# Optimization experiments

Measured on AMD Instinct MI355X. Metric: run time of the kernel, lower is better.

The kernel has to match this reference:

```python
import jax, jax.numpy as jnp
import numpy as np

N, E, D = 100000, 400000, 128
LN_EPS = 1e-5
BN_EPS = 1e-5


def layer_norm(v, g, b):
    mu = jnp.mean(v, axis=-1, keepdims=True)
    var = jnp.var(v, axis=-1, keepdims=True)
    return (v - mu) * jax.lax.rsqrt(var + LN_EPS) * g + b


def setup_inputs() -> dict:
    key = jax.random.key(0)
    ks = jax.random.split(key, 12)
    s1 = 1.0 / np.sqrt(2 * D)
    s2 = 1.0 / np.sqrt(D)
    return {
        "x": jax.random.normal(ks[0], (N, D), jnp.float32),
        "edge_attr": jax.random.normal(ks[1], (E, D), jnp.float32),
        "W1": jax.random.uniform(ks[2], (2 * D, D), jnp.float32, -s1, s1),
        "b1": jax.random.uniform(ks[3], (D,), jnp.float32, -s1, s1),
        "g1": jnp.ones((D,), jnp.float32),
        "be1": jnp.zeros((D,), jnp.float32),
        "W2": jax.random.uniform(ks[4], (D, D), jnp.float32, -s2, s2),
        "b2": jax.random.uniform(ks[5], (D,), jnp.float32, -s2, s2),
        "g2": jnp.ones((D,), jnp.float32),
        "be2": jnp.zeros((D,), jnp.float32),
        "W3": jax.random.uniform(ks[6], (D, D), jnp.float32, -s2, s2),
        "b3": jax.random.uniform(ks[7], (D,), jnp.float32, -s2, s2),
        "eps": jnp.zeros((1,), jnp.float32),
        "bn_g": jnp.ones((D,), jnp.float32),
        "bn_b": jnp.zeros((D,), jnp.float32),
        "edge_index": jax.random.randint(ks[8], (2, E), 0, N, jnp.int64),
    }


def reference(x, edge_attr, W1, b1, g1, be1, W2, b2, g2, be2, W3, b3, eps, bn_g, bn_b, edge_index):
    row, col = edge_index[0], edge_index[1]
    identity_outer = x  # in_dim == out_dim -> projections are identity
    # GIN layer
    x_j = x[row]  # [E, D] gather
    xc = jnp.concatenate([x_j, edge_attr], axis=1)  # [E, 2D]
    h = jax.nn.relu(layer_norm(xc @ W1 + b1, g1, be1))  # edge_node_mlp
    agg = jax.ops.segment_sum(h, col, num_segments=x.shape[0])  # scatter_add over col
    out = (1.0 + eps) * x + agg
    out = jax.nn.relu(layer_norm(out @ W2 + b2, g2, be2)) @ W3 + b3  # mlp
    out = out + x  # inner residual (projection is None)
    out = out + identity_outer  # outer residual
    # BatchNorm1d (training mode: batch statistics, biased var)
    mu = jnp.mean(out, axis=0)
    var = jnp.var(out, axis=0)
    out = (out - mu) * jax.lax.rsqrt(var + BN_EPS) * bn_g + bn_b
    return out
```

## Files before the change

### kernel.cpp

```cpp
#include <hip/hip_runtime.h>

#define NN 100000
#define EE 400000

typedef unsigned short u16;
typedef unsigned int u32;
typedef short short8 __attribute__((ext_vector_type(8)));
typedef __bf16 bf16x8 __attribute__((ext_vector_type(8)));
typedef float f32x4 __attribute__((ext_vector_type(4)));

__device__ __forceinline__ short8 pack_bf16x8(f32x4 lo, f32x4 hi) {
  bf16x8 r;
#pragma unroll
  for (int j = 0; j < 4; ++j) { r[j] = (__bf16)lo[j]; r[4 + j] = (__bf16)hi[j]; }
  return __builtin_bit_cast(short8, r);
}

__device__ __forceinline__ u16 f2bf(float f) {
  return __builtin_bit_cast(unsigned short, (__bf16)f);
}

__device__ __forceinline__ float bf2f(short s) {
  u32 b = ((u32)(unsigned short)s) << 16;
  return __builtin_bit_cast(float, b);
}

__global__ void __launch_bounds__(256) k_cast(
    const float* __restrict__ x, u16* __restrict__ xb)
{
  const long total = (long)NN * 16;
  for (long i = (long)blockIdx.x * 256 + threadIdx.x; i < total;
       i += (long)gridDim.x * 256) {
    f32x4 v0 = reinterpret_cast<const f32x4*>(x)[i * 2];
    f32x4 v1 = reinterpret_cast<const f32x4*>(x)[i * 2 + 1];
    reinterpret_cast<short8*>(xb)[i] = pack_bf16x8(v0, v1);
  }
}

__global__ void __launch_bounds__(256) k_hist(
    const int* __restrict__ eidx, int* __restrict__ deg)
{
  for (int e = blockIdx.x * 256 + threadIdx.x; e < EE; e += gridDim.x * 256)
    atomicAdd(&deg[eidx[EE + e]], 1);
}

__global__ void __launch_bounds__(256) k_bsum(
    const int* __restrict__ deg, int* __restrict__ bsum)
{
  const int t = threadIdx.x;
  int idx = blockIdx.x * 1024 + t * 4;
  int s = 0;
#pragma unroll
  for (int i = 0; i < 4; ++i) if (idx + i < NN) s += deg[idx + i];
#pragma unroll
  for (int m = 1; m < 64; m <<= 1) s += __shfl_xor(s, m);
  __shared__ int ws_[4];
  if ((t & 63) == 0) ws_[t >> 6] = s;
  __syncthreads();
  if (t == 0) bsum[blockIdx.x] = ws_[0] + ws_[1] + ws_[2] + ws_[3];
}

__global__ void k_scanb(int* __restrict__ bsum, int* __restrict__ start)
{
  if (threadIdx.x == 0 && blockIdx.x == 0) {
    int run = 0;
    for (int b = 0; b < 98; ++b) { int t = bsum[b]; bsum[b] = run; run += t; }
    start[NN] = EE;
  }
}

__global__ void __launch_bounds__(256) k_scanc(
    const int* __restrict__ deg, const int* __restrict__ bsum,
    int* __restrict__ start, int* __restrict__ cur)
{
  const int t = threadIdx.x, lane = t & 63, wv = t >> 6;
  int idx = blockIdx.x * 1024 + t * 4;
  int c[4], ts = 0;
#pragma unroll
  for (int i = 0; i < 4; ++i) { c[i] = (idx + i < NN) ? deg[idx + i] : 0; ts += c[i]; }
  int incl = ts;
#pragma unroll
  for (int d = 1; d < 64; d <<= 1) {
    int u = __shfl_up(incl, d);
    if (lane >= d) incl += u;
  }
  __shared__ int wsum[4];
  if (lane == 63) wsum[wv] = incl;
  __syncthreads();
  int base = bsum[blockIdx.x];
  for (int w = 0; w < wv; ++w) base += wsum[w];
  int run = base + incl - ts;
#pragma unroll
  for (int i = 0; i < 4; ++i) {
    if (idx + i < NN) { start[idx + i] = run; cur[idx + i] = run; }
    run += c[i];
  }
}

__global__ void __launch_bounds__(256) k_fill(
    const int* __restrict__ eidx, int* __restrict__ cur,
    int* __restrict__ sid, int* __restrict__ srow)
{
  for (int e = blockIdx.x * 256 + threadIdx.x; e < EE; e += gridDim.x * 256) {
    int c = eidx[EE + e];
    int p = atomicAdd(&cur[c], 1);
    sid[p] = e;
    srow[p] = eidx[e];
  }
}

__global__ void __launch_bounds__(512) k_edge(
    const u16* __restrict__ xb, const float* __restrict__ ea,
    const float* __restrict__ W1, const float* __restrict__ b1,
    const float* __restrict__ g1, const float* __restrict__ be1,
    const int* __restrict__ sid, const int* __restrict__ srow,
    u16* __restrict__ hbuf)
{
  extern __shared__ char smem[];
  const int tid = threadIdx.x;

#pragma unroll
  for (int i = 0; i < 8; ++i) {
    int f = i * 512 + tid;
    int lo_ = f & 15;
    int kb_ = (f >> 4) & 3;
    int kc_ = (f >> 6) & 7;
    int nt_ = f >> 9;
    int n = nt_ * 16 + lo_;
    int k0 = kc_ * 32 + kb_ * 8;
    bf16x8 p;
#pragma unroll
    for (int j = 0; j < 8; ++j) p[j] = (__bf16)W1[(k0 + j) * 128 + n];
    *reinterpret_cast<short8*>(smem + f * 16) = __builtin_bit_cast(short8, p);
  }

  const int lane = tid & 63;
  const int wv = tid >> 6;
  const int lo = lane & 15;
  const int kb = lane >> 4;
  char* tb = smem + 65536 + wv * 1024;

  float b1v[8], g1v[8], bev[8];
#pragma unroll
  for (int nt = 0; nt < 8; ++nt) {
    int c = nt * 16 + lo;
    b1v[nt] = b1[c]; g1v[nt] = g1[c]; bev[nt] = be1[c];
  }
  __syncthreads();

  for (int t = blockIdx.x; t < EE / 128; t += gridDim.x) {
    const int pbase = t * 128 + wv * 16;
    const int p = pbase + lo;
    const int e = sid[p];
    const int r = srow[p];

    short8 a[8];
#pragma unroll
    for (int kc = 0; kc < 4; ++kc)
      a[kc] = *reinterpret_cast<const short8*>(xb + (long)r * 128 + kc * 32 + kb * 8);
#pragma unroll
    for (int kc = 4; kc < 8; ++kc) {
      const float* src = ea + (long)e * 128 + (kc - 4) * 32 + kb * 8;
      f32x4 v0 = __builtin_nontemporal_load(reinterpret_cast<const f32x4*>(src));
      f32x4 v1 = __builtin_nontemporal_load(reinterpret_cast<const f32x4*>(src) + 1);
      a[kc] = pack_bf16x8(v0, v1);
    }

    f32x4 acc[8];
#pragma unroll
    for (int nt = 0; nt < 8; ++nt) acc[nt] = (f32x4){0.f, 0.f, 0.f, 0.f};

#pragma unroll
    for (int nt = 0; nt < 8; ++nt)
#pragma unroll
      for (int kc = 0; kc < 8; ++kc) {
        short8 b = *reinterpret_cast<const short8*>(
            smem + nt * 8192 + kc * 1024 + lane * 16);
        acc[nt] = __builtin_amdgcn_mfma_f32_16x16x32_bf16(a[kc], b, acc[nt], 0, 0, 0);
      }

    float s[4] = {0.f, 0.f, 0.f, 0.f};
    float q[4] = {0.f, 0.f, 0.f, 0.f};
#pragma unroll
    for (int nt = 0; nt < 8; ++nt)
#pragma unroll
      for (int i = 0; i < 4; ++i) {
        float v = acc[nt][i] + b1v[nt];
        acc[nt][i] = v;
        s[i] += v; q[i] += v * v;
      }
#pragma unroll
    for (int m = 1; m < 16; m <<= 1)
#pragma unroll
      for (int i = 0; i < 4; ++i) {
        s[i] += __shfl_xor(s[i], m);
        q[i] += __shfl_xor(q[i], m);
      }
    float mu[4], rs[4];
#pragma unroll
    for (int i = 0; i < 4; ++i) {
      mu[i] = s[i] * (1.f / 128.f);
      float var = q[i] * (1.f / 128.f) - mu[i] * mu[i];
      rs[i] = rsqrtf(var + 1e-5f);
    }

    u32 pk[8][4];
#pragma unroll
    for (int nt = 0; nt < 8; ++nt)
#pragma unroll
      for (int i = 0; i < 4; ++i) {
        float v = fmaxf((acc[nt][i] - mu[i]) * rs[i] * g1v[nt] + bev[nt], 0.f);
        float vn = __shfl_xor(v, 1);
        pk[nt][i] = (u32)f2bf(v) | ((u32)f2bf(vn) << 16);
      }

#pragma unroll
    for (int h = 0; h < 4; ++h) {
      if (h) asm volatile("s_waitcnt lgkmcnt(0)" ::: "memory");
      if (kb == h && !(lo & 1)) {
#pragma unroll
        for (int nt = 0; nt < 8; ++nt)
#pragma unroll
          for (int i = 0; i < 4; ++i)
            *reinterpret_cast<u32*>(tb + i * 256 + (nt * 16 + lo) * 2) = pk[nt][i];
      }
      short8 rv = *reinterpret_cast<const short8*>(
          tb + (lane >> 4) * 256 + (lane & 15) * 16);
      __builtin_nontemporal_store(rv,
          reinterpret_cast<short8*>(hbuf + ((long)pbase + h * 4 + (lane >> 4)) * 128
                                    + (lane & 15) * 8));
    }
  }
}

__global__ void __launch_bounds__(256) k_node1(
    const u16* __restrict__ xb, const u16* __restrict__ hbuf,
    const int* __restrict__ start,
    const float* __restrict__ W2, const float* __restrict__ b2,
    const float* __restrict__ g2, const float* __restrict__ be2,
    const float* __restrict__ epsp, u16* __restrict__ t1)
{
  __shared__ char smem[32768];
  const int tid = threadIdx.x;
#pragma unroll
  for (int i = 0; i < 8; ++i) {
    int f = i * 256 + tid;
    int lo_ = f & 15;
    int kb_ = (f >> 4) & 3;
    int kc_ = (f >> 6) & 3;
    int nt_ = f >> 8;
    int n = nt_ * 16 + lo_;
    int k0 = kc_ * 32 + kb_ * 8;
    bf16x8 p;
#pragma unroll
    for (int j = 0; j < 8; ++j) p[j] = (__bf16)W2[(k0 + j) * 128 + n];
    *reinterpret_cast<short8*>(smem + f * 16) = __builtin_bit_cast(short8, p);
  }

  const int lane = tid & 63, wv = tid >> 6, lo = lane & 15, kb = lane >> 4;
  const float ope = 1.f + epsp[0];
  __syncthreads();

  const int row = blockIdx.x * 64 + wv * 16 + lo;
  const int n = row < NN ? row : NN - 1;

  float uacc[4][8];
#pragma unroll
  for (int kc = 0; kc < 4; ++kc)
#pragma unroll
    for (int j = 0; j < 8; ++j) uacc[kc][j] = 0.f;

  const int p0 = start[n], p1 = start[n + 1];
  int p = p0;
  for (; p + 2 <= p1; p += 2) {
    const u16* h0 = hbuf + (long)p * 128 + kb * 8;
    short8 hv0[4], hv1[4];
#pragma unroll
    for (int kc = 0; kc < 4; ++kc) {
      hv0[kc] = __builtin_nontemporal_load(reinterpret_cast<const short8*>(h0 + kc * 32));
      hv1[kc] = __builtin_nontemporal_load(reinterpret_cast<const short8*>(h0 + 128 + kc * 32));
    }
#pragma unroll
    for (int kc = 0; kc < 4; ++kc)
#pragma unroll
      for (int j = 0; j < 8; ++j)
        uacc[kc][j] += bf2f(hv0[kc][j]) + bf2f(hv1[kc][j]);
  }
  if (p < p1) {
    const u16* h0 = hbuf + (long)p * 128 + kb * 8;
#pragma unroll
    for (int kc = 0; kc < 4; ++kc) {
      short8 hv = __builtin_nontemporal_load(reinterpret_cast<const short8*>(h0 + kc * 32));
#pragma unroll
      for (int j = 0; j < 8; ++j) uacc[kc][j] += bf2f(hv[j]);
    }
  }

  short8 a[4];
#pragma unroll
  for (int kc = 0; kc < 4; ++kc) {
    short8 xv = *reinterpret_cast<const short8*>(xb + (long)n * 128 + kc * 32 + kb * 8);
    f32x4 u0, u1;
#pragma unroll
    for (int j = 0; j < 4; ++j) {
      u0[j] = fmaf(bf2f(xv[j]), ope, uacc[kc][j]);
      u1[j] = fmaf(bf2f(xv[4 + j]), ope, uacc[kc][4 + j]);
    }
    a[kc] = pack_bf16x8(u0, u1);
  }

  f32x4 acc[8];
#pragma unroll
  for (int nt = 0; nt < 8; ++nt) acc[nt] = (f32x4){0.f, 0.f, 0.f, 0.f};

#pragma unroll
  for (int nt = 0; nt < 8; ++nt)
#pragma unroll
    for (int kc = 0; kc < 4; ++kc) {
      short8 b = *reinterpret_cast<const short8*>(smem + nt * 4096 + kc * 1024 + lane * 16);
      acc[nt] = __builtin_amdgcn_mfma_f32_16x16x32_bf16(a[kc], b, acc[nt], 0, 0, 0);
    }

  float b2v[8], g2v[8], bev[8];
#pragma unroll
  for (int nt = 0; nt < 8; ++nt) {
    int c = nt * 16 + lo;
    b2v[nt] = b2[c]; g2v[nt] = g2[c]; bev[nt] = be2[c];
  }

  float s[4] = {0.f, 0.f, 0.f, 0.f};
  float q[4] = {0.f, 0.f, 0.f, 0.f};
#pragma unroll
  for (int nt = 0; nt < 8; ++nt)
#pragma unroll
    for (int i = 0; i < 4; ++i) {
      float v = acc[nt][i] + b2v[nt];
      acc[nt][i] = v;
      s[i] += v; q[i] += v * v;
    }
#pragma unroll
  for (int m = 1; m < 16; m <<= 1)
#pragma unroll
    for (int i = 0; i < 4; ++i) {
      s[i] += __shfl_xor(s[i], m);
      q[i] += __shfl_xor(q[i], m);
    }
  float mu[4], rs[4];
  int rows[4];
#pragma unroll
  for (int i = 0; i < 4; ++i) {
    mu[i] = s[i] * (1.f / 128.f);
    float var = q[i] * (1.f / 128.f) - mu[i] * mu[i];
    rs[i] = rsqrtf(var + 1e-5f);
    int idx = blockIdx.x * 64 + wv * 16 + kb * 4 + i;
    rows[i] = idx < NN ? idx : -1;
  }
#pragma unroll
  for (int nt = 0; nt < 8; ++nt)
#pragma unroll
    for (int i = 0; i < 4; ++i) {
      float v = fmaxf((acc[nt][i] - mu[i]) * rs[i] * g2v[nt] + bev[nt], 0.f);
      float vn = __shfl_xor(v, 1);
      if (!(lo & 1) && rows[i] >= 0) {
        u32 pk = (u32)f2bf(v) | ((u32)f2bf(vn) << 16);
        *reinterpret_cast<u32*>(t1 + (long)rows[i] * 128 + nt * 16 + lo) = pk;
      }
    }
}

__global__ void __launch_bounds__(256) k_node2(
    const u16* __restrict__ t1, const float* __restrict__ x,
    const float* __restrict__ W3, const float* __restrict__ b3,
    u16* __restrict__ tmp, float* __restrict__ part)
{
  __shared__ char smem[32768];
  const int tid = threadIdx.x;
#pragma unroll
  for (int i = 0; i < 8; ++i) {
    int f = i * 256 + tid;
    int lo_ = f & 15;
    int kb_ = (f >> 4) & 3;
    int kc_ = (f >> 6) & 3;
    int nt_ = f >> 8;
    int n = nt_ * 16 + lo_;
    int k0 = kc_ * 32 + kb_ * 8;
    bf16x8 p;
#pragma unroll
    for (int j = 0; j < 8; ++j) p[j] = (__bf16)W3[(k0 + j) * 128 + n];
    *reinterpret_cast<short8*>(smem + f * 16) = __builtin_bit_cast(short8, p);
  }
  __syncthreads();

  const int lane = tid & 63, wv = tid >> 6, lo = lane & 15, kb = lane >> 4;
  const long rb = (long)blockIdx.x * 128 + wv * 32;

  short8 a[2][4];
#pragma unroll
  for (int mt = 0; mt < 2; ++mt) {
    long row = rb + mt * 16 + lo;
    long rc = row < NN ? row : (NN - 1);
#pragma unroll
    for (int kc = 0; kc < 4; ++kc)
      a[mt][kc] = *reinterpret_cast<const short8*>(t1 + rc * 128 + kc * 32 + kb * 8);
  }

  f32x4 acc[2][8];
#pragma unroll
  for (int mt = 0; mt < 2; ++mt)
#pragma unroll
    for (int nt = 0; nt < 8; ++nt)
      acc[mt][nt] = (f32x4){0.f, 0.f, 0.f, 0.f};

#pragma unroll
  for (int nt = 0; nt < 8; ++nt)
#pragma unroll
    for (int kc = 0; kc < 4; ++kc) {
      short8 b = *reinterpret_cast<const short8*>(smem + nt * 4096 + kc * 1024 + lane * 16);
      acc[0][nt] = __builtin_amdgcn_mfma_f32_16x16x32_bf16(a[0][kc], b, acc[0][nt], 0, 0, 0);
      acc[1][nt] = __builtin_amdgcn_mfma_f32_16x16x32_bf16(a[1][kc], b, acc[1][nt], 0, 0, 0);
    }

  float b3v[8];
#pragma unroll
  for (int nt = 0; nt < 8; ++nt) b3v[nt] = b3[nt * 16 + lo];

  float sn[8] = {0.f, 0.f, 0.f, 0.f, 0.f, 0.f, 0.f, 0.f};
  float qn[8] = {0.f, 0.f, 0.f, 0.f, 0.f, 0.f, 0.f, 0.f};

#pragma unroll
  for (int mt = 0; mt < 2; ++mt) {
    long rows[4], rc[4];
    bool val[4];
#pragma unroll
    for (int i = 0; i < 4; ++i) {
      rows[i] = rb + mt * 16 + kb * 4 + i;
      val[i] = rows[i] < NN;
      rc[i] = val[i] ? rows[i] : (NN - 1);
    }
#pragma unroll
    for (int nt = 0; nt < 8; ++nt)
#pragma unroll
      for (int i = 0; i < 4; ++i) {
        float v = acc[mt][nt][i] + b3v[nt] + 2.f * x[rc[i] * 128 + nt * 16 + lo];
        if (val[i]) { sn[nt] += v; qn[nt] += v * v; }
        float vn = __shfl_xor(v, 1);
        if (!(lo & 1) && val[i]) {
          u32 pk = (u32)f2bf(v) | ((u32)f2bf(vn) << 16);
          *reinterpret_cast<u32*>(tmp + rows[i] * 128 + nt * 16 + lo) = pk;
        }
      }
  }
#pragma unroll
  for (int nt = 0; nt < 8; ++nt) {
    sn[nt] += __shfl_xor(sn[nt], 16); sn[nt] += __shfl_xor(sn[nt], 32);
    qn[nt] += __shfl_xor(qn[nt], 16); qn[nt] += __shfl_xor(qn[nt], 32);
  }
  if (lane < 16) {
    long pr = ((long)blockIdx.x * 4 + wv) * 256;
#pragma unroll
    for (int nt = 0; nt < 8; ++nt) {
      part[pr + nt * 16 + lane] = sn[nt];
      part[pr + 128 + nt * 16 + lane] = qn[nt];
    }
  }
}

__global__ void __launch_bounds__(256) k_stats(
    const float* __restrict__ part, const float* __restrict__ bng,
    const float* __restrict__ bnb, float* __restrict__ stats2)
{
  const int c = blockIdx.x;
  const int tid = threadIdx.x;
  float s = 0.f, q = 0.f;
  for (int i = tid; i < 3128; i += 256) {
    s += part[(long)i * 256 + c];
    q += part[(long)i * 256 + 128 + c];
  }
#pragma unroll
  for (int m = 1; m < 64; m <<= 1) { s += __shfl_xor(s, m); q += __shfl_xor(q, m); }
  __shared__ float rs_[4], rq_[4];
  const int wv = tid >> 6;
  if ((tid & 63) == 0) { rs_[wv] = s; rq_[wv] = q; }
  __syncthreads();
  if (tid == 0) {
    s = rs_[0] + rs_[1] + rs_[2] + rs_[3];
    q = rq_[0] + rq_[1] + rq_[2] + rq_[3];
    float mu = s * (1.f / (float)NN);
    float var = q * (1.f / (float)NN) - mu * mu;
    float sc = rsqrtf(var + 1e-5f) * bng[c];
    stats2[c] = sc;
    stats2[128 + c] = bnb[c] - mu * sc;
  }
}

__global__ void __launch_bounds__(256) k_apply(
    const u16* __restrict__ tmp, const float* __restrict__ stats2,
    float* __restrict__ out)
{
  const long total = (long)NN * 16;
  for (long i = (long)blockIdx.x * 256 + threadIdx.x; i < total;
       i += (long)gridDim.x * 256) {
    int db = (int)((i & 15) << 3);
    short8 hv = reinterpret_cast<const short8*>(tmp)[i];
    f32x4 sc0 = *reinterpret_cast<const f32x4*>(stats2 + db);
    f32x4 sc1 = *reinterpret_cast<const f32x4*>(stats2 + db + 4);
    f32x4 sh0 = *reinterpret_cast<const f32x4*>(stats2 + 128 + db);
    f32x4 sh1 = *reinterpret_cast<const f32x4*>(stats2 + 128 + db + 4);
    f32x4 o0, o1;
#pragma unroll
    for (int j = 0; j < 4; ++j) {
      o0[j] = fmaf(bf2f(hv[j]), sc0[j], sh0[j]);
      o1[j] = fmaf(bf2f(hv[4 + j]), sc1[j], sh1[j]);
    }
    reinterpret_cast<f32x4*>(out)[i * 2] = o0;
    reinterpret_cast<f32x4*>(out)[i * 2 + 1] = o1;
  }
}

extern "C" void kernel_launch(void* const* d_in, const int* in_sizes, int n_in,
                              void* d_out, int out_size, void* d_ws, size_t ws_size,
                              hipStream_t stream)
{
  const float* x   = (const float*)d_in[0];
  const float* ea  = (const float*)d_in[1];
  const float* W1  = (const float*)d_in[2];
  const float* b1  = (const float*)d_in[3];
  const float* g1  = (const float*)d_in[4];
  const float* be1 = (const float*)d_in[5];
  const float* W2  = (const float*)d_in[6];
  const float* b2  = (const float*)d_in[7];
  const float* g2  = (const float*)d_in[8];
  const float* be2 = (const float*)d_in[9];
  const float* W3  = (const float*)d_in[10];
  const float* b3  = (const float*)d_in[11];
  const float* eps = (const float*)d_in[12];
  const float* bng = (const float*)d_in[13];
  const float* bnb = (const float*)d_in[14];
  const int*   eidx = (const int*)d_in[15];
  float* out = (float*)d_out;

  u16*   hbuf   = (u16*)d_ws;
  u16*   t1     = (u16*)((char*)d_ws + 102400000L);
  u16*   xb     = (u16*)((char*)d_ws + 128000000L);
  u16*   tmp    = (u16*)d_ws;
  float* part   = (float*)((char*)d_ws + 153600000L);
  float* stats2 = part + 3128L * 256;
  int*   deg    = (int*)(stats2 + 256);
  int*   start  = deg + NN;
  int*   cur    = start + NN + 1;
  int*   bsum   = cur + NN;
  int*   sid    = bsum + 128;
  int*   srow   = sid + EE;

  (void)hipFuncSetAttribute(reinterpret_cast<const void*>(k_edge),
                            hipFuncAttributeMaxDynamicSharedMemorySize, 73728);

  hipMemsetAsync(deg, 0, (size_t)NN * 4, stream);
  k_cast  <<<1024, 256, 0, stream>>>(x, xb);
  k_hist  <<<512, 256, 0, stream>>>(eidx, deg);
  k_bsum  <<<98, 256, 0, stream>>>(deg, bsum);
  k_scanb <<<1, 64, 0, stream>>>(bsum, start);
  k_scanc <<<98, 256, 0, stream>>>(deg, bsum, start, cur);
  k_fill  <<<512, 256, 0, stream>>>(eidx, cur, sid, srow);
  k_edge  <<<512, 512, 73728, stream>>>(xb, ea, W1, b1, g1, be1, sid, srow, hbuf);
  k_node1 <<<(NN + 63) / 64, 256, 0, stream>>>(xb, hbuf, start, W2, b2, g2, be2, eps, t1);
  k_node2 <<<(NN + 127) / 128, 256, 0, stream>>>(t1, x, W3, b3, tmp, part);
  k_stats <<<128, 256, 0, stream>>>(part, bng, bnb, stats2);
  k_apply <<<2048, 256, 0, stream>>>(tmp, stats2, out);
}
```

Measured before the change: 276.5 us.

## Fuse scatter-add into edge kernel via fp32 atomics, drop per-edge h buffer

The edge kernel no longer writes each edge's bf16 hidden row to a staging buffer for the node kernel to segment-reduce. It now reduces runs of consecutive sorted edges that share a destination in registers and issues fp32 atomicAdds into a node-level aggregate buffer. That buffer is zeroed by a new kernel, and the node kernel reads it directly. This removes the write and re-read of a roughly 100MB intermediate, in exchange for zeroing a 51MB fp32 buffer and many global atomics, which also make the summation order nondeterministic.

```diff
diff --git a/kernel.cpp b/kernel.cpp
--- a/kernel.cpp
+++ b/kernel.cpp
@@ -23,6 +23,16 @@
 __device__ __forceinline__ float bf2f(short s) {
   u32 b = ((u32)(unsigned short)s) << 16;
   return __builtin_bit_cast(float, b);
+}
+
+__global__ void __launch_bounds__(256) k_zero(
+    float* __restrict__ agg, int* __restrict__ deg)
+{
+  const long stride = (long)gridDim.x * 256;
+  const long i0 = (long)blockIdx.x * 256 + threadIdx.x;
+  for (long i = i0; i < (long)NN * 32; i += stride)
+    reinterpret_cast<f32x4*>(agg)[i] = (f32x4){0.f, 0.f, 0.f, 0.f};
+  for (long i = i0; i < NN; i += stride) deg[i] = 0;
 }
 
 __global__ void __launch_bounds__(256) k_cast(
@@ -99,13 +109,14 @@
 
 __global__ void __launch_bounds__(256) k_fill(
     const int* __restrict__ eidx, int* __restrict__ cur,
-    int* __restrict__ sid, int* __restrict__ srow)
+    int* __restrict__ sid, int* __restrict__ srow, int* __restrict__ ncol)
 {
   for (int e = blockIdx.x * 256 + threadIdx.x; e < EE; e += gridDim.x * 256) {
     int c = eidx[EE + e];
     int p = atomicAdd(&cur[c], 1);
     sid[p] = e;
     srow[p] = eidx[e];
+    ncol[p] = c;
   }
 }
 
@@ -114,7 +125,7 @@
     const float* __restrict__ W1, const float* __restrict__ b1,
     const float* __restrict__ g1, const float* __restrict__ be1,
     const int* __restrict__ sid, const int* __restrict__ srow,
-    u16* __restrict__ hbuf)
+    const int* __restrict__ ncol, float* __restrict__ agg)
 {
   extern __shared__ char smem[];
   const int tid = threadIdx.x;
@@ -138,7 +149,6 @@
   const int wv = tid >> 6;
   const int lo = lane & 15;
   const int kb = lane >> 4;
-  char* tb = smem + 65536 + wv * 1024;
 
   float b1v[8], g1v[8], bev[8];
 #pragma unroll
@@ -154,6 +164,9 @@
     const int e = sid[p];
     const int r = srow[p];
 
+    int4 ndv = *reinterpret_cast<const int4*>(ncol + pbase + kb * 4);
+    int nd[4] = {ndv.x, ndv.y, ndv.z, ndv.w};
+
     short8 a[8];
 #pragma unroll
     for (int kc = 0; kc < 4; ++kc)
@@ -204,38 +217,32 @@
       rs[i] = rsqrtf(var + 1e-5f);
     }
 
-    u32 pk[8][4];
 #pragma unroll
     for (int nt = 0; nt < 8; ++nt)
 #pragma unroll
-      for (int i = 0; i < 4; ++i) {
-        float v = fmaxf((acc[nt][i] - mu[i]) * rs[i] * g1v[nt] + bev[nt], 0.f);
-        float vn = __shfl_xor(v, 1);
-        pk[nt][i] = (u32)f2bf(v) | ((u32)f2bf(vn) << 16);
+      for (int i = 0; i < 4; ++i)
+        acc[nt][i] = fmaxf((acc[nt][i] - mu[i]) * rs[i] * g1v[nt] + bev[nt], 0.f);
+
+#pragma unroll
+    for (int nt = 0; nt < 8; ++nt) {
+      const int c = nt * 16 + lo;
+      float rsum = acc[nt][0];
+#pragma unroll
+      for (int i = 1; i < 4; ++i) {
+        if (nd[i] == nd[i - 1]) {
+          rsum += acc[nt][i];
+        } else {
+          atomicAdd(agg + (long)nd[i - 1] * 128 + c, rsum);
+          rsum = acc[nt][i];
+        }
       }
-
-#pragma unroll
-    for (int h = 0; h < 4; ++h) {
-      if (h) asm volatile("s_waitcnt lgkmcnt(0)" ::: "memory");
-      if (kb == h && !(lo & 1)) {
-#pragma unroll
-        for (int nt = 0; nt < 8; ++nt)
-#pragma unroll
-          for (int i = 0; i < 4; ++i)
-            *reinterpret_cast<u32*>(tb + i * 256 + (nt * 16 + lo) * 2) = pk[nt][i];
-      }
-      short8 rv = *reinterpret_cast<const short8*>(
-          tb + (lane >> 4) * 256 + (lane & 15) * 16);
-      __builtin_nontemporal_store(rv,
-          reinterpret_cast<short8*>(hbuf + ((long)pbase + h * 4 + (lane >> 4)) * 128
-                                    + (lane & 15) * 8));
+      atomicAdd(agg + (long)nd[3] * 128 + c, rsum);
     }
   }
 }
 
 __global__ void __launch_bounds__(256) k_node1(
-    const u16* __restrict__ xb, const u16* __restrict__ hbuf,
-    const int* __restrict__ start,
+    const u16* __restrict__ xb, const float* __restrict__ agg,
     const float* __restrict__ W2, const float* __restrict__ b2,
     const float* __restrict__ g2, const float* __restrict__ be2,
     const float* __restrict__ epsp, u16* __restrict__ t1)
@@ -264,47 +271,18 @@
   const int row = blockIdx.x * 64 + wv * 16 + lo;
   const int n = row < NN ? row : NN - 1;
 
-  float uacc[4][8];
-#pragma unroll
-  for (int kc = 0; kc < 4; ++kc)
-#pragma unroll
-    for (int j = 0; j < 8; ++j) uacc[kc][j] = 0.f;
-
-  const int p0 = start[n], p1 = start[n + 1];
-  int p = p0;
-  for (; p + 2 <= p1; p += 2) {
-    const u16* h0 = hbuf + (long)p * 128 + kb * 8;
-    short8 hv0[4], hv1[4];
-#pragma unroll
-    for (int kc = 0; kc < 4; ++kc) {
-      hv0[kc] = __builtin_nontemporal_load(reinterpret_cast<const short8*>(h0 + kc * 32));
-      hv1[kc] = __builtin_nontemporal_load(reinterpret_cast<const short8*>(h0 + 128 + kc * 32));
-    }
-#pragma unroll
-    for (int kc = 0; kc < 4; ++kc)
-#pragma unroll
-      for (int j = 0; j < 8; ++j)
-        uacc[kc][j] += bf2f(hv0[kc][j]) + bf2f(hv1[kc][j]);
-  }
-  if (p < p1) {
-    const u16* h0 = hbuf + (long)p * 128 + kb * 8;
-#pragma unroll
-    for (int kc = 0; kc < 4; ++kc) {
-      short8 hv = __builtin_nontemporal_load(reinterpret_cast<const short8*>(h0 + kc * 32));
-#pragma unroll
-      for (int j = 0; j < 8; ++j) uacc[kc][j] += bf2f(hv[j]);
-    }
-  }
-
   short8 a[4];
 #pragma unroll
   for (int kc = 0; kc < 4; ++kc) {
+    const float* gp = agg + (long)n * 128 + kc * 32 + kb * 8;
+    f32x4 g0 = *reinterpret_cast<const f32x4*>(gp);
+    f32x4 g1 = *reinterpret_cast<const f32x4*>(gp + 4);
     short8 xv = *reinterpret_cast<const short8*>(xb + (long)n * 128 + kc * 32 + kb * 8);
     f32x4 u0, u1;
 #pragma unroll
     for (int j = 0; j < 4; ++j) {
-      u0[j] = fmaf(bf2f(xv[j]), ope, uacc[kc][j]);
-      u1[j] = fmaf(bf2f(xv[4 + j]), ope, uacc[kc][4 + j]);
+      u0[j] = fmaf(bf2f(xv[j]), ope, g0[j]);
+      u1[j] = fmaf(bf2f(xv[4 + j]), ope, g1[j]);
     }
     a[kc] = pack_bf16x8(u0, u1);
   }
@@ -539,10 +517,10 @@
   const int*   eidx = (const int*)d_in[15];
   float* out = (float*)d_out;
 
-  u16*   hbuf   = (u16*)d_ws;
+  u16*   tmp    = (u16*)d_ws;
+  float* agg    = (float*)((char*)d_ws + 25600000L);
   u16*   t1     = (u16*)((char*)d_ws + 102400000L);
   u16*   xb     = (u16*)((char*)d_ws + 128000000L);
-  u16*   tmp    = (u16*)d_ws;
   float* part   = (float*)((char*)d_ws + 153600000L);
   float* stats2 = part + 3128L * 256;
   int*   deg    = (int*)(stats2 + 256);
@@ -551,19 +529,20 @@
   int*   bsum   = cur + NN;
   int*   sid    = bsum + 128;
   int*   srow   = sid + EE;
+  int*   ncol   = srow + EE;
 
   (void)hipFuncSetAttribute(reinterpret_cast<const void*>(k_edge),
-                            hipFuncAttributeMaxDynamicSharedMemorySize, 73728);
-
-  hipMemsetAsync(deg, 0, (size_t)NN * 4, stream);
+                            hipFuncAttributeMaxDynamicSharedMemorySize, 65536);
+
+  k_zero  <<<2048, 256, 0, stream>>>(agg, deg);
   k_cast  <<<1024, 256, 0, stream>>>(x, xb);
   k_hist  <<<512, 256, 0, stream>>>(eidx, deg);
   k_bsum  <<<98, 256, 0, stream>>>(deg, bsum);
   k_scanb <<<1, 64, 0, stream>>>(bsum, start);
   k_scanc <<<98, 256, 0, stream>>>(deg, bsum, start, cur);
-  k_fill  <<<512, 256, 0, stream>>>(eidx, cur, sid, srow);
-  k_edge  <<<512, 512, 73728, stream>>>(xb, ea, W1, b1, g1, be1, sid, srow, hbuf);
-  k_node1 <<<(NN + 63) / 64, 256, 0, stream>>>(xb, hbuf, start, W2, b2, g2, be2, eps, t1);
+  k_fill  <<<512, 256, 0, stream>>>(eidx, cur, sid, srow, ncol);
+  k_edge  <<<512, 512, 65536, stream>>>(xb, ea, W1, b1, g1, be1, sid, srow, ncol, agg);
+  k_node1 <<<(NN + 63) / 64, 256, 0, stream>>>(xb, agg, W2, b2, g2, be2, eps, t1);
   k_node2 <<<(NN + 127) / 128, 256, 0, stream>>>(t1, x, W3, b3, tmp, part);
   k_stats <<<128, 256, 0, stream>>>(part, bng, bnb, stats2);
   k_apply <<<2048, 256, 0, stream>>>(tmp, stats2, out);
```

Result: slower. 459.2 us (+66.1%).

## Aggregate CSR edge rows per wave cooperatively into LDS in node1

Applied to the files above, without the earlier changes.

Replaces the per-lane segmented reduction, where each lane walked its own node's edge list reading 16-byte chunks, with a wave-cooperative sweep. The wave walks the contiguous edge range of its 16 nodes, and each lane sums two columns. It flushes the partial sums into a per-wave LDS tile whenever the destination column changes, using a new ncol array written by k_fill. This gives coalesced 256-byte row reads and avoids the load imbalance from skewed degrees within a wave. In exchange it adds an extra ncol read per edge, a write in k_fill, serial per-edge iteration within each wave, and about 66 KB of LDS per block, which may reduce occupancy.

```diff
diff --git a/kernel.cpp b/kernel.cpp
--- a/kernel.cpp
+++ b/kernel.cpp
@@ -8,6 +8,7 @@
 typedef short short8 __attribute__((ext_vector_type(8)));
 typedef __bf16 bf16x8 __attribute__((ext_vector_type(8)));
 typedef float f32x4 __attribute__((ext_vector_type(4)));
+typedef float f32x2 __attribute__((ext_vector_type(2)));
 
 __device__ __forceinline__ short8 pack_bf16x8(f32x4 lo, f32x4 hi) {
   bf16x8 r;
@@ -99,13 +100,14 @@
 
 __global__ void __launch_bounds__(256) k_fill(
     const int* __restrict__ eidx, int* __restrict__ cur,
-    int* __restrict__ sid, int* __restrict__ srow)
+    int* __restrict__ sid, int* __restrict__ srow, int* __restrict__ ncol)
 {
   for (int e = blockIdx.x * 256 + threadIdx.x; e < EE; e += gridDim.x * 256) {
     int c = eidx[EE + e];
     int p = atomicAdd(&cur[c], 1);
     sid[p] = e;
     srow[p] = eidx[e];
+    ncol[p] = c;
   }
 }
 
@@ -235,12 +237,12 @@
 
 __global__ void __launch_bounds__(256) k_node1(
     const u16* __restrict__ xb, const u16* __restrict__ hbuf,
-    const int* __restrict__ start,
+    const int* __restrict__ start, const int* __restrict__ ncol,
     const float* __restrict__ W2, const float* __restrict__ b2,
     const float* __restrict__ g2, const float* __restrict__ be2,
     const float* __restrict__ epsp, u16* __restrict__ t1)
 {
-  __shared__ char smem[32768];
+  extern __shared__ char smem[];
   const int tid = threadIdx.x;
 #pragma unroll
   for (int i = 0; i < 8; ++i) {
@@ -259,53 +261,53 @@
 
   const int lane = tid & 63, wv = tid >> 6, lo = lane & 15, kb = lane >> 4;
   const float ope = 1.f + epsp[0];
+  float* aggw = reinterpret_cast<float*>(smem + 32768) + wv * 2080;
+
+#pragma unroll
+  for (int nl = 0; nl < 16; ++nl)
+    *reinterpret_cast<f32x2*>(aggw + nl * 130 + 2 * lane) = (f32x2){0.f, 0.f};
+
   __syncthreads();
+
+  const int nb = blockIdx.x * 64 + wv * 16;
+  const int nlo = nb < NN ? nb : NN;
+  const int nhi = (nb + 16) < NN ? (nb + 16) : NN;
+  int p = start[nlo];
+  const int p1 = start[nhi];
+  float r0 = 0.f, r1 = 0.f;
+  for (; p < p1; ++p) {
+    u32 hv = *reinterpret_cast<const u32*>(hbuf + (long)p * 128 + 2 * lane);
+    int nc = ncol[p];
+    r0 += bf2f((short)(hv & 0xffff));
+    r1 += bf2f((short)(hv >> 16));
+    bool fl = (p + 1 >= p1) || (ncol[p + 1] != nc);
+    if (fl) {
+      *reinterpret_cast<f32x2*>(aggw + (nc - nb) * 130 + 2 * lane) = (f32x2){r0, r1};
+      r0 = 0.f; r1 = 0.f;
+    }
+  }
 
   const int row = blockIdx.x * 64 + wv * 16 + lo;
   const int n = row < NN ? row : NN - 1;
 
-  float uacc[4][8];
-#pragma unroll
-  for (int kc = 0; kc < 4; ++kc)
-#pragma unroll
-    for (int j = 0; j < 8; ++j) uacc[kc][j] = 0.f;
-
-  const int p0 = start[n], p1 = start[n + 1];
-  int p = p0;
-  for (; p + 2 <= p1; p += 2) {
-    const u16* h0 = hbuf + (long)p * 128 + kb * 8;
-    short8 hv0[4], hv1[4];
-#pragma unroll
-    for (int kc = 0; kc < 4; ++kc) {
-      hv0[kc] = __builtin_nontemporal_load(reinterpret_cast<const short8*>(h0 + kc * 32));
-      hv1[kc] = __builtin_nontemporal_load(reinterpret_cast<const short8*>(h0 + 128 + kc * 32));
-    }
-#pragma unroll
-    for (int kc = 0; kc < 4; ++kc)
-#pragma unroll
-      for (int j = 0; j < 8; ++j)
-        uacc[kc][j] += bf2f(hv0[kc][j]) + bf2f(hv1[kc][j]);
-  }
-  if (p < p1) {
-    const u16* h0 = hbuf + (long)p * 128 + kb * 8;
-#pragma unroll
-    for (int kc = 0; kc < 4; ++kc) {
-      short8 hv = __builtin_nontemporal_load(reinterpret_cast<const short8*>(h0 + kc * 32));
-#pragma unroll
-      for (int j = 0; j < 8; ++j) uacc[kc][j] += bf2f(hv[j]);
-    }
-  }
-
   short8 a[4];
 #pragma unroll
   for (int kc = 0; kc < 4; ++kc) {
+    const float* gp = aggw + lo * 130 + kc * 32 + kb * 8;
+    f32x2 q0 = *reinterpret_cast<const f32x2*>(gp);
+    f32x2 q1 = *reinterpret_cast<const f32x2*>(gp + 2);
+    f32x2 q2 = *reinterpret_cast<const f32x2*>(gp + 4);
+    f32x2 q3 = *reinterpret_cast<const f32x2*>(gp + 6);
     short8 xv = *reinterpret_cast<const short8*>(xb + (long)n * 128 + kc * 32 + kb * 8);
     f32x4 u0, u1;
-#pragma unroll
-    for (int j = 0; j < 4; ++j) {
-      u0[j] = fmaf(bf2f(xv[j]), ope, uacc[kc][j]);
-      u1[j] = fmaf(bf2f(xv[4 + j]), ope, uacc[kc][4 + j]);
-    }
+    u0[0] = fmaf(bf2f(xv[0]), ope, q0[0]);
+    u0[1] = fmaf(bf2f(xv[1]), ope, q0[1]);
+    u0[2] = fmaf(bf2f(xv[2]), ope, q1[0]);
+    u0[3] = fmaf(bf2f(xv[3]), ope, q1[1]);
+    u1[0] = fmaf(bf2f(xv[4]), ope, q2[0]);
+    u1[1] = fmaf(bf2f(xv[5]), ope, q2[1]);
+    u1[2] = fmaf(bf2f(xv[6]), ope, q3[0]);
+    u1[3] = fmaf(bf2f(xv[7]), ope, q3[1]);
     a[kc] = pack_bf16x8(u0, u1);
   }
 
@@ -540,9 +542,9 @@
   float* out = (float*)d_out;
 
   u16*   hbuf   = (u16*)d_ws;
+  u16*   tmp    = (u16*)d_ws;
   u16*   t1     = (u16*)((char*)d_ws + 102400000L);
   u16*   xb     = (u16*)((char*)d_ws + 128000000L);
-  u16*   tmp    = (u16*)d_ws;
   float* part   = (float*)((char*)d_ws + 153600000L);
   float* stats2 = part + 3128L * 256;
   int*   deg    = (int*)(stats2 + 256);
@@ -551,9 +553,12 @@
   int*   bsum   = cur + NN;
   int*   sid    = bsum + 128;
   int*   srow   = sid + EE;
+  int*   ncol   = srow + EE;
 
   (void)hipFuncSetAttribute(reinterpret_cast<const void*>(k_edge),
                             hipFuncAttributeMaxDynamicSharedMemorySize, 73728);
+  (void)hipFuncSetAttribute(reinterpret_cast<const void*>(k_node1),
+                            hipFuncAttributeMaxDynamicSharedMemorySize, 66048);
 
   hipMemsetAsync(deg, 0, (size_t)NN * 4, stream);
   k_cast  <<<1024, 256, 0, stream>>>(x, xb);
@@ -561,9 +566,10 @@
   k_bsum  <<<98, 256, 0, stream>>>(deg, bsum);
   k_scanb <<<1, 64, 0, stream>>>(bsum, start);
   k_scanc <<<98, 256, 0, stream>>>(deg, bsum, start, cur);
-  k_fill  <<<512, 256, 0, stream>>>(eidx, cur, sid, srow);
+  k_fill  <<<512, 256, 0, stream>>>(eidx, cur, sid, srow, ncol);
   k_edge  <<<512, 512, 73728, stream>>>(xb, ea, W1, b1, g1, be1, sid, srow, hbuf);
-  k_node1 <<<(NN + 63) / 64, 256, 0, stream>>>(xb, hbuf, start, W2, b2, g2, be2, eps, t1);
+  k_node1 <<<(NN + 63) / 64, 256, 66048, stream>>>(xb, hbuf, start, ncol,
+                                                   W2, b2, g2, be2, eps, t1);
   k_node2 <<<(NN + 127) / 128, 256, 0, stream>>>(t1, x, W3, b3, tmp, part);
   k_stats <<<128, 256, 0, stream>>>(part, bng, bnb, stats2);
   k_apply <<<2048, 256, 0, stream>>>(tmp, stats2, out);
```

Measured after the change: 413.2 us. +49.5%, slower.

## Move edge aggregation into an edge-parallel segmented-reduction kernel

Applied to the files above, without the earlier changes.

Aggregation of edge messages moves out of the node MLP kernel into a new kernel that walks the CSR-sorted edge buffer in fixed chunks of 64 edges. Each chunk does a segmented sum in shared memory and writes whole segments to an fp32 agg buffer, using atomics only for the boundary segments. The goal is to remove load imbalance and per-thread sequential loops over variable-degree neighbour lists in k_node1. The cost is an extra 51 MB fp32 buffer that has to be zeroed, written and re-read, plus one more kernel launch and an extra ncol array.

```diff
diff --git a/kernel.cpp b/kernel.cpp
--- a/kernel.cpp
+++ b/kernel.cpp
@@ -2,10 +2,12 @@
 
 #define NN 100000
 #define EE 400000
+#define RPB 64
 
 typedef unsigned short u16;
 typedef unsigned int u32;
 typedef short short8 __attribute__((ext_vector_type(8)));
+typedef short short4v __attribute__((ext_vector_type(4)));
 typedef __bf16 bf16x8 __attribute__((ext_vector_type(8)));
 typedef float f32x4 __attribute__((ext_vector_type(4)));
 
@@ -23,6 +25,16 @@
 __device__ __forceinline__ float bf2f(short s) {
   u32 b = ((u32)(unsigned short)s) << 16;
   return __builtin_bit_cast(float, b);
+}
+
+__global__ void __launch_bounds__(256) k_zero(
+    float* __restrict__ agg, int* __restrict__ deg)
+{
+  const long stride = (long)gridDim.x * 256;
+  const long i0 = (long)blockIdx.x * 256 + threadIdx.x;
+  for (long i = i0; i < (long)NN * 32; i += stride)
+    reinterpret_cast<f32x4*>(agg)[i] = (f32x4){0.f, 0.f, 0.f, 0.f};
+  for (long i = i0; i < NN; i += stride) deg[i] = 0;
 }
 
 __global__ void __launch_bounds__(256) k_cast(
@@ -99,13 +111,14 @@
 
 __global__ void __launch_bounds__(256) k_fill(
     const int* __restrict__ eidx, int* __restrict__ cur,
-    int* __restrict__ sid, int* __restrict__ srow)
+    int* __restrict__ sid, int* __restrict__ srow, int* __restrict__ ncol)
 {
   for (int e = blockIdx.x * 256 + threadIdx.x; e < EE; e += gridDim.x * 256) {
     int c = eidx[EE + e];
     int p = atomicAdd(&cur[c], 1);
     sid[p] = e;
     srow[p] = eidx[e];
+    ncol[p] = c;
   }
 }
 
@@ -233,9 +246,75 @@
   }
 }
 
+__global__ void __launch_bounds__(256) k_agg(
+    const u16* __restrict__ hbuf, const int* __restrict__ ncol,
+    float* __restrict__ agg)
+{
+  __shared__ float accs[RPB][128];
+  __shared__ int ncols[RPB];
+  __shared__ int segid[RPB];
+  __shared__ int segnode[RPB];
+  __shared__ int nsegS;
+
+  const int tid = threadIdx.x;
+  const int p0 = blockIdx.x * RPB;
+
+#pragma unroll
+  for (int i = 0; i < 8; ++i)
+    reinterpret_cast<f32x4*>(&accs[0][0])[i * 256 + tid] = (f32x4){0.f, 0.f, 0.f, 0.f};
+  if (tid < RPB) ncols[tid] = ncol[p0 + tid];
+  __syncthreads();
+
+  if (tid < 64) {
+    int flag = (tid == 0) ? 0 : (ncols[tid] != ncols[tid - 1] ? 1 : 0);
+    int incl = flag;
+#pragma unroll
+    for (int d = 1; d < 64; d <<= 1) {
+      int u = __shfl_up(incl, d);
+      if (tid >= d) incl += u;
+    }
+    segid[tid] = incl;
+    if (flag || tid == 0) segnode[incl] = ncols[tid];
+    if (tid == 63) nsegS = incl + 1;
+  }
+  __syncthreads();
+
+  const int rg = tid >> 5;
+  const int cs = tid & 31;
+  float run[4] = {0.f, 0.f, 0.f, 0.f};
+  int curseg = segid[rg * 8];
+#pragma unroll
+  for (int i = 0; i < 8; ++i) {
+    int r = rg * 8 + i;
+    int sg = segid[r];
+    short4v hv = __builtin_nontemporal_load(
+        reinterpret_cast<const short4v*>(hbuf + (long)(p0 + r) * 128 + cs * 4));
+    if (sg != curseg) {
+#pragma unroll
+      for (int j = 0; j < 4; ++j) atomicAdd(&accs[curseg][cs * 4 + j], run[j]);
+#pragma unroll
+      for (int j = 0; j < 4; ++j) run[j] = 0.f;
+      curseg = sg;
+    }
+#pragma unroll
+    for (int j = 0; j < 4; ++j) run[j] += bf2f(hv[j]);
+  }
+#pragma unroll
+  for (int j = 0; j < 4; ++j) atomicAdd(&accs[curseg][cs * 4 + j], run[j]);
+  __syncthreads();
+
+  const int nseg = nsegS;
+  const int c = tid & 127;
+  for (int s = tid >> 7; s < nseg; s += 2) {
+    float v = accs[s][c];
+    long a = (long)segnode[s] * 128 + c;
+    if (s == 0 || s == nseg - 1) atomicAdd(&agg[a], v);
+    else agg[a] = v;
+  }
+}
+
 __global__ void __launch_bounds__(256) k_node1(
-    const u16* __restrict__ xb, const u16* __restrict__ hbuf,
-    const int* __restrict__ start,
+    const u16* __restrict__ xb, const float* __restrict__ agg,
     const float* __restrict__ W2, const float* __restrict__ b2,
     const float* __restrict__ g2, const float* __restrict__ be2,
     const float* __restrict__ epsp, u16* __restrict__ t1)
@@ -264,47 +343,18 @@
   const int row = blockIdx.x * 64 + wv * 16 + lo;
   const int n = row < NN ? row : NN - 1;
 
-  float uacc[4][8];
-#pragma unroll
-  for (int kc = 0; kc < 4; ++kc)
-#pragma unroll
-    for (int j = 0; j < 8; ++j) uacc[kc][j] = 0.f;
-
-  const int p0 = start[n], p1 = start[n + 1];
-  int p = p0;
-  for (; p + 2 <= p1; p += 2) {
-    const u16* h0 = hbuf + (long)p * 128 + kb * 8;
-    short8 hv0[4], hv1[4];
-#pragma unroll
-    for (int kc = 0; kc < 4; ++kc) {
-      hv0[kc] = __builtin_nontemporal_load(reinterpret_cast<const short8*>(h0 + kc * 32));
-      hv1[kc] = __builtin_nontemporal_load(reinterpret_cast<const short8*>(h0 + 128 + kc * 32));
-    }
-#pragma unroll
-    for (int kc = 0; kc < 4; ++kc)
-#pragma unroll
-      for (int j = 0; j < 8; ++j)
-        uacc[kc][j] += bf2f(hv0[kc][j]) + bf2f(hv1[kc][j]);
-  }
-  if (p < p1) {
-    const u16* h0 = hbuf + (long)p * 128 + kb * 8;
-#pragma unroll
-    for (int kc = 0; kc < 4; ++kc) {
-      short8 hv = __builtin_nontemporal_load(reinterpret_cast<const short8*>(h0 + kc * 32));
-#pragma unroll
-      for (int j = 0; j < 8; ++j) uacc[kc][j] += bf2f(hv[j]);
-    }
-  }
-
   short8 a[4];
 #pragma unroll
   for (int kc = 0; kc < 4; ++kc) {
+    const float* gp = agg + (long)n * 128 + kc * 32 + kb * 8;
+    f32x4 g0 = *reinterpret_cast<const f32x4*>(gp);
+    f32x4 g1 = *reinterpret_cast<const f32x4*>(gp + 4);
     short8 xv = *reinterpret_cast<const short8*>(xb + (long)n * 128 + kc * 32 + kb * 8);
     f32x4 u0, u1;
 #pragma unroll
     for (int j = 0; j < 4; ++j) {
-      u0[j] = fmaf(bf2f(xv[j]), ope, uacc[kc][j]);
-      u1[j] = fmaf(bf2f(xv[4 + j]), ope, uacc[kc][4 + j]);
+      u0[j] = fmaf(bf2f(xv[j]), ope, g0[j]);
+      u1[j] = fmaf(bf2f(xv[4 + j]), ope, g1[j]);
     }
     a[kc] = pack_bf16x8(u0, u1);
   }
@@ -540,10 +590,11 @@
   float* out = (float*)d_out;
 
   u16*   hbuf   = (u16*)d_ws;
+  u16*   tmp    = (u16*)d_ws;
   u16*   t1     = (u16*)((char*)d_ws + 102400000L);
   u16*   xb     = (u16*)((char*)d_ws + 128000000L);
-  u16*   tmp    = (u16*)d_ws;
-  float* part   = (float*)((char*)d_ws + 153600000L);
+  float* agg    = (float*)((char*)d_ws + 153600000L);
+  float* part   = (float*)((char*)d_ws + 204800000L);
   float* stats2 = part + 3128L * 256;
   int*   deg    = (int*)(stats2 + 256);
   int*   start  = deg + NN;
@@ -551,19 +602,21 @@
   int*   bsum   = cur + NN;
   int*   sid    = bsum + 128;
   int*   srow   = sid + EE;
+  int*   ncol   = srow + EE;
 
   (void)hipFuncSetAttribute(reinterpret_cast<const void*>(k_edge),
                             hipFuncAttributeMaxDynamicSharedMemorySize, 73728);
 
-  hipMemsetAsync(deg, 0, (size_t)NN * 4, stream);
+  k_zero  <<<2048, 256, 0, stream>>>(agg, deg);
   k_cast  <<<1024, 256, 0, stream>>>(x, xb);
   k_hist  <<<512, 256, 0, stream>>>(eidx, deg);
   k_bsum  <<<98, 256, 0, stream>>>(deg, bsum);
   k_scanb <<<1, 64, 0, stream>>>(bsum, start);
   k_scanc <<<98, 256, 0, stream>>>(deg, bsum, start, cur);
-  k_fill  <<<512, 256, 0, stream>>>(eidx, cur, sid, srow);
+  k_fill  <<<512, 256, 0, stream>>>(eidx, cur, sid, srow, ncol);
   k_edge  <<<512, 512, 73728, stream>>>(xb, ea, W1, b1, g1, be1, sid, srow, hbuf);
-  k_node1 <<<(NN + 63) / 64, 256, 0, stream>>>(xb, hbuf, start, W2, b2, g2, be2, eps, t1);
+  k_agg   <<<EE / RPB, 256, 0, stream>>>(hbuf, ncol, agg);
+  k_node1 <<<(NN + 63) / 64, 256, 0, stream>>>(xb, agg, W2, b2, g2, be2, eps, t1);
   k_node2 <<<(NN + 127) / 128, 256, 0, stream>>>(t1, x, W3, b3, tmp, part);
   k_stats <<<128, 256, 0, stream>>>(part, bng, bnb, stats2);
   k_apply <<<2048, 256, 0, stream>>>(tmp, stats2, out);
```

Result: slower. 364.1 us (+31.7%).
